# Kernel tuning notes

Hardware: AMD Instinct MI355X
Metric: run time of the kernel (lower is better)

## Reference

```python
import jax, jax.numpy as jnp
import numpy as np

HEAD_DIM = 64
N_HEADS = 12
N_KV_HEADS = 4
N_REP = N_HEADS // N_KV_HEADS  # 3


def _rope(x, cos, sin):
    # x: [B, S, H, D]; cos/sin: [1, S, D//2] -> broadcast over heads
    x2 = x.reshape(*x.shape[:-1], -1, 2)          # [B,S,H,D/2,2]
    x_r, x_i = x2[..., 0], x2[..., 1]
    c = cos[:, :, None, :]                         # [1,S,1,D/2]
    s = sin[:, :, None, :]
    o_r = x_r * c - x_i * s
    o_i = x_r * s + x_i * c
    return jnp.stack([o_r, o_i], axis=-1).reshape(x.shape)


def setup_inputs() -> dict:
    key = jax.random.key(0)
    ks = jax.random.split(key, 6)
    B, S, H = 4, 2048, 768
    hidden_state = jax.random.normal(ks[0], (B, S, H), dtype=jnp.float32)
    # true RoPE frequencies (theta=10000) for positions 0..S-1
    inv_freq = 1.0 / (10000.0 ** (np.arange(0, HEAD_DIM, 2, dtype=np.float32) / HEAD_DIM))
    ang = np.arange(S, dtype=np.float32)[:, None] * inv_freq[None, :]  # [S, D/2]
    freqs_cos = jnp.asarray(np.cos(ang))[None]     # [1,S,32]
    freqs_sin = jnp.asarray(np.sin(ang))[None]
    sc = 0.02
    wq = jax.random.normal(ks[1], (768, 768), dtype=jnp.float32) * sc
    wk = jax.random.normal(ks[2], (256, 768), dtype=jnp.float32) * sc
    wv = jax.random.normal(ks[3], (256, 768), dtype=jnp.float32) * sc
    wo = jax.random.normal(ks[4], (768, 768), dtype=jnp.float32) * sc
    return {"hidden_state": hidden_state, "freqs_cos": freqs_cos, "freqs_sin": freqs_sin,
            "wq": wq, "wk": wk, "wv": wv, "wo": wo}


def reference(hidden_state, freqs_cos, freqs_sin, wq, wk, wv, wo):
    B, S, _ = hidden_state.shape
    q = (hidden_state @ wq.T).reshape(B, S, N_HEADS, HEAD_DIM)
    k = (hidden_state @ wk.T).reshape(B, S, N_KV_HEADS, HEAD_DIM)
    v = (hidden_state @ wv.T).reshape(B, S, N_KV_HEADS, HEAD_DIM)
    q = _rope(q, freqs_cos, freqs_sin)
    k = _rope(k, freqs_cos, freqs_sin)
    # repeat_kv: [B,S,KV,D] -> [B,S,KV*n_rep,D]
    k = jnp.repeat(k, N_REP, axis=2)
    v = jnp.repeat(v, N_REP, axis=2)
    q = q.transpose(0, 2, 1, 3)  # [B,H,S,D]
    k = k.transpose(0, 2, 1, 3)
    v = v.transpose(0, 2, 1, 3)
    scores = jnp.einsum('bhqd,bhkd->bhqk', q, k) / np.sqrt(HEAD_DIM).astype(np.float32)
    mask = jnp.triu(jnp.full((S, S), -jnp.inf, dtype=scores.dtype), k=1)
    scores = scores + mask
    attn = jax.nn.softmax(scores.astype(jnp.float32), axis=-1).astype(q.dtype)
    # dropout is inference-off (identity)
    out = jnp.einsum('bhqk,bhkd->bhqd', attn, v)
    out = out.transpose(0, 2, 1, 3).reshape(B, S, N_HEADS * HEAD_DIM)
    return out @ wo.T, attn
```

## Files before the change

kernel.cpp:

```cpp
#include <hip/hip_runtime.h>
#include <hip/hip_bf16.h>
#include <stdint.h>


typedef __bf16 bf16x8 __attribute__((ext_vector_type(8)));
typedef float  f32x4  __attribute__((ext_vector_type(4)));

#define B_    4
#define S_    2048
#define H_    768
#define NH_Q  12
#define NKV_  4
#define D_    64
#define MROWS (B_ * S_)
#define NQKV  1280

__device__ __forceinline__ f32x4 mfma16(bf16x8 a, bf16x8 b, f32x4 c) {
  return __builtin_amdgcn_mfma_f32_16x16x32_bf16(a, b, c, 0, 0, 0);
}

__device__ __forceinline__ void st_nt4(float* p, f32x4 v) {
  __builtin_nontemporal_store(v, (f32x4*)p);
}

__device__ __forceinline__ uint32_t pk2(float a, float b) {
  __bf16 x = (__bf16)a, y = (__bf16)b;
  uint16_t xu = __builtin_bit_cast(uint16_t, x);
  uint16_t yu = __builtin_bit_cast(uint16_t, y);
  return (uint32_t)xu | ((uint32_t)yu << 16);
}
__device__ __forceinline__ float bl(uint32_t u) {
  uint32_t t = u << 16; return __builtin_bit_cast(float, t);
}
__device__ __forceinline__ float bh(uint32_t u) {
  uint32_t t = u & 0xffff0000u; return __builtin_bit_cast(float, t);
}

__global__ void cast_bf16_kernel(const float* __restrict__ s, __bf16* __restrict__ d, int n8) {
  int i = blockIdx.x * 256 + threadIdx.x;
  if (i >= n8) return;
  const float4* sp = (const float4*)s + (size_t)i * 2;
  float4 a = sp[0], b = sp[1];
  bf16x8 o;
  o[0] = (__bf16)a.x; o[1] = (__bf16)a.y; o[2] = (__bf16)a.z; o[3] = (__bf16)a.w;
  o[4] = (__bf16)b.x; o[5] = (__bf16)b.y; o[6] = (__bf16)b.z; o[7] = (__bf16)b.w;
  *((bf16x8*)d + i) = o;
}

__global__ __launch_bounds__(256) void gemm_qkv(const __bf16* __restrict__ A,
                                                const __bf16* __restrict__ Wq,
                                                const __bf16* __restrict__ Wk,
                                                const __bf16* __restrict__ Wv,
                                                float* __restrict__ C) {
  const int K = 768;
  __shared__ __bf16 As[128 * 32];
  __shared__ __bf16 Bs[128 * 32];
  const int m0 = blockIdx.x * 128, n0 = blockIdx.y * 128;
  const __bf16* W;
  int nl;
  if (n0 < 768)       { W = Wq; nl = n0; }
  else if (n0 < 1024) { W = Wk; nl = n0 - 768; }
  else                { W = Wv; nl = n0 - 1024; }
  const int tid = threadIdx.x, lane = tid & 63, w = tid >> 6;
  const int wm = w >> 1, wn = w & 1;
  const int ql = lane & 15, grp = lane >> 4;
  const int srow = tid >> 1, shalf = tid & 1;
  const int sw = (srow >> 1) & 3;
  const int kc0 = (shalf * 2) ^ sw, kc1 = (shalf * 2 + 1) ^ sw;

  f32x4 acc[4][4] = {};

  for (int k0 = 0; k0 < K; k0 += 32) {
    bf16x8 av0 = *(const bf16x8*)(A + (size_t)(m0 + srow) * K + k0 + shalf * 16);
    bf16x8 av1 = *(const bf16x8*)(A + (size_t)(m0 + srow) * K + k0 + shalf * 16 + 8);
    bf16x8 bv0 = *(const bf16x8*)(W + (size_t)(nl + srow) * K + k0 + shalf * 16);
    bf16x8 bv1 = *(const bf16x8*)(W + (size_t)(nl + srow) * K + k0 + shalf * 16 + 8);
    __syncthreads();
    *(bf16x8*)(As + srow * 32 + kc0 * 8) = av0;
    *(bf16x8*)(As + srow * 32 + kc1 * 8) = av1;
    *(bf16x8*)(Bs + srow * 32 + kc0 * 8) = bv0;
    *(bf16x8*)(Bs + srow * 32 + kc1 * 8) = bv1;
    __syncthreads();

    bf16x8 af[4], bf_[4];
#pragma unroll
    for (int i = 0; i < 4; i++) {
      int row = wm * 64 + i * 16 + ql;
      int kc = grp ^ ((row >> 1) & 3);
      af[i] = *(const bf16x8*)(As + row * 32 + kc * 8);
    }
#pragma unroll
    for (int j = 0; j < 4; j++) {
      int row = wn * 64 + j * 16 + ql;
      int kc = grp ^ ((row >> 1) & 3);
      bf_[j] = *(const bf16x8*)(Bs + row * 32 + kc * 8);
    }
#pragma unroll
    for (int i = 0; i < 4; i++)
#pragma unroll
      for (int j = 0; j < 4; j++)
        acc[i][j] = mfma16(af[i], bf_[j], acc[i][j]);
  }

#pragma unroll
  for (int i = 0; i < 4; i++)
#pragma unroll
    for (int j = 0; j < 4; j++)
#pragma unroll
      for (int r = 0; r < 4; r++) {
        int row = m0 + wm * 64 + i * 16 + grp * 4 + r;
        int col = n0 + wn * 64 + j * 16 + ql;
        C[(size_t)row * NQKV + col] = acc[i][j][r];
      }
}

__global__ __launch_bounds__(256) void gemm_xwT(const __bf16* __restrict__ A,
                                                const __bf16* __restrict__ W,
                                                float* __restrict__ C,
                                                int M, int N, int K) {
  __shared__ __bf16 As[128 * 32];
  __shared__ __bf16 Bs[128 * 32];
  const int m0 = blockIdx.x * 128, n0 = blockIdx.y * 128;
  const int tid = threadIdx.x, lane = tid & 63, w = tid >> 6;
  const int wm = w >> 1, wn = w & 1;
  const int ql = lane & 15, grp = lane >> 4;
  const int srow = tid >> 1, shalf = tid & 1;
  const int sw = (srow >> 1) & 3;
  const int kc0 = (shalf * 2) ^ sw, kc1 = (shalf * 2 + 1) ^ sw;

  f32x4 acc[4][4] = {};

  for (int k0 = 0; k0 < K; k0 += 32) {
    bf16x8 av0 = *(const bf16x8*)(A + (size_t)(m0 + srow) * K + k0 + shalf * 16);
    bf16x8 av1 = *(const bf16x8*)(A + (size_t)(m0 + srow) * K + k0 + shalf * 16 + 8);
    bf16x8 bv0 = *(const bf16x8*)(W + (size_t)(n0 + srow) * K + k0 + shalf * 16);
    bf16x8 bv1 = *(const bf16x8*)(W + (size_t)(n0 + srow) * K + k0 + shalf * 16 + 8);
    __syncthreads();
    *(bf16x8*)(As + srow * 32 + kc0 * 8) = av0;
    *(bf16x8*)(As + srow * 32 + kc1 * 8) = av1;
    *(bf16x8*)(Bs + srow * 32 + kc0 * 8) = bv0;
    *(bf16x8*)(Bs + srow * 32 + kc1 * 8) = bv1;
    __syncthreads();

    bf16x8 af[4], bf_[4];
#pragma unroll
    for (int i = 0; i < 4; i++) {
      int row = wm * 64 + i * 16 + ql;
      int kc = grp ^ ((row >> 1) & 3);
      af[i] = *(const bf16x8*)(As + row * 32 + kc * 8);
    }
#pragma unroll
    for (int j = 0; j < 4; j++) {
      int row = wn * 64 + j * 16 + ql;
      int kc = grp ^ ((row >> 1) & 3);
      bf_[j] = *(const bf16x8*)(Bs + row * 32 + kc * 8);
    }
#pragma unroll
    for (int i = 0; i < 4; i++)
#pragma unroll
      for (int j = 0; j < 4; j++)
        acc[i][j] = mfma16(af[i], bf_[j], acc[i][j]);
  }

#pragma unroll
  for (int i = 0; i < 4; i++)
#pragma unroll
    for (int j = 0; j < 4; j++)
#pragma unroll
      for (int r = 0; r < 4; r++) {
        int row = m0 + wm * 64 + i * 16 + grp * 4 + r;
        int col = n0 + wn * 64 + j * 16 + ql;
        C[(size_t)row * N + col] = acc[i][j][r];
      }
}

template <int NH>
__global__ void rope_pack(const float* __restrict__ src, int colOff, int stride,
                          const float* __restrict__ fc, const float* __restrict__ fs,
                          __bf16* __restrict__ dst, float scale) {
  int idx = blockIdx.x * 256 + threadIdx.x;
  const int total = MROWS * NH * 32;
  if (idx >= total) return;
  int t = idx & 31;
  int h = (idx >> 5) % NH;
  int row = idx / (32 * NH);
  int s = row & (S_ - 1), b = row >> 11;
  float x0 = src[(size_t)row * stride + colOff + h * 64 + 2 * t];
  float x1 = src[(size_t)row * stride + colOff + h * 64 + 2 * t + 1];
  float c = fc[s * 32 + t], sn = fs[s * 32 + t];
  float o0 = (x0 * c - x1 * sn) * scale;
  float o1 = (x0 * sn + x1 * c) * scale;
  __bf16* d = dst + (((size_t)(b * NH + h) * S_ + s) * 64 + 2 * t);
  d[0] = (__bf16)o0;
  d[1] = (__bf16)o1;
}

__global__ void transpose_v(const float* __restrict__ QKV, __bf16* __restrict__ VT) {
  __shared__ float tile[64][65];
  int rt = blockIdx.x;
  int ct = blockIdx.y;
  int r0 = rt * 64, c0 = ct * 64;
  int tx = threadIdx.x & 63, ty = threadIdx.x >> 6;
#pragma unroll
  for (int rep = 0; rep < 16; rep++) {
    int rr = rep * 4 + ty;
    tile[rr][tx] = QKV[(size_t)(r0 + rr) * NQKV + 1024 + c0 + tx];
  }
  __syncthreads();
  int b = r0 >> 11;
  int s0 = r0 & (S_ - 1);
#pragma unroll
  for (int rep = 0; rep < 16; rep++) {
    int dr = rep * 4 + ty;
    int d = c0 + dr;
    int kv = d >> 6, dd = d & 63;
    VT[(((size_t)(b * NKV_ + kv) * 64 + dd) * S_) + s0 + tx] = (__bf16)tile[tx][dr];
  }
}

template <int MAXC>
__device__ __forceinline__ void attn_part(
    int g, int b, int h, int w, int lane,
    const __bf16* __restrict__ Q, const __bf16* __restrict__ Kp,
    const __bf16* __restrict__ Vp, float* __restrict__ attn,
    __bf16* __restrict__ O, float (*lsum_s)[16], f32x4 (*obuf)[4]) {
  const int ql = lane & 15, grp = lane >> 4;
  const int qr0 = g * 16;
  const int nch = (g >> 1) + 1;
  const int i_q = qr0 + ql;
  const __bf16* Qp = Q + ((size_t)(b * NH_Q + h) * S_ + qr0) * 64;
  float* attnp = attn + ((size_t)(b * NH_Q + h) * S_ + qr0) * S_;

  bf16x8 bq0 = *(const bf16x8*)(Qp + ql * 64 + grp * 8);
  bf16x8 bq1 = *(const bf16x8*)(Qp + ql * 64 + 32 + grp * 8);

  uint32_t p[MAXC][4];
  float lsum = 0.f;

#pragma unroll
  for (int c = 0; c < MAXC; c++) {
    const int j = w + 4 * c;
    if (j < nch) {
      const int j0 = j * 32;
      bf16x8 k0 = *(const bf16x8*)(Kp + (size_t)(j0 + ql) * 64 + grp * 8);
      bf16x8 k1 = *(const bf16x8*)(Kp + (size_t)(j0 + ql) * 64 + 32 + grp * 8);
      bf16x8 k2 = *(const bf16x8*)(Kp + (size_t)(j0 + 16 + ql) * 64 + grp * 8);
      bf16x8 k3 = *(const bf16x8*)(Kp + (size_t)(j0 + 16 + ql) * 64 + 32 + grp * 8);
      f32x4 s0 = {}, s1 = {};
      s0 = mfma16(k0, bq0, s0);
      s0 = mfma16(k1, bq1, s0);
      s1 = mfma16(k2, bq0, s1);
      s1 = mfma16(k3, bq1, s1);
      float e[8];
      if (j == nch - 1) {
#pragma unroll
        for (int r = 0; r < 4; r++) {
          int ja = j0 + grp * 4 + r, jb = j0 + 16 + grp * 4 + r;
          e[r]     = (ja <= i_q) ? exp2f(s0[r]) : 0.f;
          e[4 + r] = (jb <= i_q) ? exp2f(s1[r]) : 0.f;
        }
      } else {
#pragma unroll
        for (int r = 0; r < 4; r++) {
          e[r]     = exp2f(s0[r]);
          e[4 + r] = exp2f(s1[r]);
        }
      }
#pragma unroll
      for (int r = 0; r < 8; r++) lsum += e[r];
      p[c][0] = pk2(e[0], e[1]);
      p[c][1] = pk2(e[2], e[3]);
      p[c][2] = pk2(e[4], e[5]);
      p[c][3] = pk2(e[6], e[7]);
    }
  }

  lsum += __shfl_xor(lsum, 16);
  lsum += __shfl_xor(lsum, 32);
  if (lane < 16) lsum_s[w][ql] = lsum;
  __syncthreads();
  const float rinv = 1.f / (lsum_s[0][ql] + lsum_s[1][ql] + lsum_s[2][ql] + lsum_s[3][ql]);

  f32x4 opv[4] = {};
#pragma unroll
  for (int c = 0; c < MAXC; c++) {
    const int j = w + 4 * c;
    if (j < nch) {
      const int j0 = j * 32;
      bf16x8 v0 = *(const bf16x8*)(Vp + (size_t)(0 * 16 + ql) * S_ + j0 + grp * 8);
      bf16x8 v1 = *(const bf16x8*)(Vp + (size_t)(1 * 16 + ql) * S_ + j0 + grp * 8);
      bf16x8 v2 = *(const bf16x8*)(Vp + (size_t)(2 * 16 + ql) * S_ + j0 + grp * 8);
      bf16x8 v3 = *(const bf16x8*)(Vp + (size_t)(3 * 16 + ql) * S_ + j0 + grp * 8);

      f32x4 q0, q1;
      q0[0] = bl(p[c][0]); q0[1] = bh(p[c][0]); q0[2] = bl(p[c][1]); q0[3] = bh(p[c][1]);
      q1[0] = bl(p[c][2]); q1[1] = bh(p[c][2]); q1[2] = bl(p[c][3]); q1[3] = bh(p[c][3]);
#pragma unroll
      for (int r = 0; r < 4; r++) { q0[r] *= rinv; q1[r] *= rinv; }
      st_nt4(attnp + (size_t)ql * S_ + j0 + grp * 4, q0);
      st_nt4(attnp + (size_t)ql * S_ + j0 + 16 + grp * 4, q1);

      int srcA = ql + 32 * (grp & 1);
      int srcB = srcA + 16;
      uint32_t A0 = __shfl(p[c][0], srcA), A1 = __shfl(p[c][1], srcA);
      uint32_t A2 = __shfl(p[c][2], srcA), A3 = __shfl(p[c][3], srcA);
      uint32_t B0 = __shfl(p[c][0], srcB), B1 = __shfl(p[c][1], srcB);
      uint32_t B2 = __shfl(p[c][2], srcB), B3 = __shfl(p[c][3], srcB);
      bool hi = (grp >> 1) != 0;
      union { bf16x8 v; uint32_t u[4]; } pu;
      pu.u[0] = hi ? A2 : A0;
      pu.u[1] = hi ? A3 : A1;
      pu.u[2] = hi ? B2 : B0;
      pu.u[3] = hi ? B3 : B1;
      opv[0] = mfma16(pu.v, v0, opv[0]);
      opv[1] = mfma16(pu.v, v1, opv[1]);
      opv[2] = mfma16(pu.v, v2, opv[2]);
      opv[3] = mfma16(pu.v, v3, opv[3]);
    }
  }

  f32x4* ob = obuf[w * 64 + lane];
  ob[0] = opv[0]; ob[1] = opv[1]; ob[2] = opv[2]; ob[3] = opv[3];
  __syncthreads();
  {
    const int dt = w;
    f32x4 acc = obuf[0 * 64 + lane][dt];
    acc += obuf[1 * 64 + lane][dt];
    acc += obuf[2 * 64 + lane][dt];
    acc += obuf[3 * 64 + lane][dt];
    __bf16* Op = O + ((size_t)(b * S_) + qr0) * H_ + h * 64;
#pragma unroll
    for (int r = 0; r < 4; r++) {
      int row = grp * 4 + r;
      float rr = 1.f / (lsum_s[0][row] + lsum_s[1][row] + lsum_s[2][row] + lsum_s[3][row]);
      Op[(size_t)row * H_ + dt * 16 + ql] = (__bf16)(acc[r] * rr);
    }
  }

  const int jz = nch * 32;
  const int tid = w * 64 + lane;
  const f32x4 z4 = {0.f, 0.f, 0.f, 0.f};
#pragma unroll 1
  for (int rr = 0; rr < 16; rr++) {
    float* rowp = attnp + (size_t)rr * S_;
    for (int jj = jz + tid * 4; jj < S_; jj += 1024) st_nt4(rowp + jj, z4);
  }
  __syncthreads();
}

__global__ __launch_bounds__(256) void attn_kernel(const __bf16* __restrict__ Q,
                                                   const __bf16* __restrict__ Kb,
                                                   const __bf16* __restrict__ VT,
                                                   float* __restrict__ attn,
                                                   __bf16* __restrict__ O) {
  __shared__ float lsum_s[4][16];
  __shared__ f32x4 obuf[4 * 64][4];
  const int x = blockIdx.x, h = blockIdx.y, b = blockIdx.z;
  const int lane = threadIdx.x & 63, w = threadIdx.x >> 6;
  const int kv = h / 3;
  const __bf16* Kp = Kb + (size_t)(b * NKV_ + kv) * S_ * 64;
  const __bf16* Vp = VT + (size_t)(b * NKV_ + kv) * 64 * S_;

  attn_part<8>(x, b, h, w, lane, Q, Kp, Vp, attn, O, lsum_s, obuf);
  attn_part<16>(127 - x, b, h, w, lane, Q, Kp, Vp, attn, O, lsum_s, obuf);
}

extern "C" void kernel_launch(void* const* d_in, const int* in_sizes, int n_in,
                              void* d_out, int out_size, void* d_ws, size_t ws_size,
                              hipStream_t stream) {
  (void)in_sizes; (void)n_in;
  const float* X  = (const float*)d_in[0];
  const float* fc = (const float*)d_in[1];
  const float* fs = (const float*)d_in[2];
  const float* wq = (const float*)d_in[3];
  const float* wk = (const float*)d_in[4];
  const float* wv = (const float*)d_in[5];
  const float* wo = (const float*)d_in[6];
  float* out0 = (float*)d_out;
  float* attn = out0 + (size_t)B_ * S_ * H_;

  char* p = (char*)d_ws;
  auto take = [&](size_t bytes) -> char* {
    char* r = p;
    p += (bytes + 255) & ~(size_t)255;
    return r;
  };
  __bf16* wqbf = (__bf16*)take((size_t)768 * 768 * 2);
  __bf16* wkbf = (__bf16*)take((size_t)256 * 768 * 2);
  __bf16* wvbf = (__bf16*)take((size_t)256 * 768 * 2);
  __bf16* wobf = (__bf16*)take((size_t)768 * 768 * 2);
  __bf16* Qbf  = (__bf16*)take((size_t)MROWS * 768 * 2);
  __bf16* Kbf  = (__bf16*)take((size_t)MROWS * 256 * 2);
  __bf16* VTbf = (__bf16*)take((size_t)MROWS * 256 * 2);
  __bf16* Obf  = (__bf16*)take((size_t)MROWS * 768 * 2);
  size_t used = (size_t)(p - (char*)d_ws);

  const size_t XBF_B  = (size_t)MROWS * 768 * 2;
  const size_t QKV_B  = (size_t)MROWS * NQKV * 4;
  const size_t TEMP_B = XBF_B + QKV_B;

  char* tp;
  if (used + TEMP_B + 1024 <= ws_size) {
    tp = p;
  } else {
    tp = (char*)(((uintptr_t)((char*)d_out + (size_t)out_size * 4 - TEMP_B)) & ~(uintptr_t)255);
  }
  __bf16* Xbf  = (__bf16*)tp;  tp += XBF_B;
  float*  QKVf = (float*)tp;

  {
    int n8;
    n8 = (MROWS * 768) / 8;
    cast_bf16_kernel<<<(n8 + 255) / 256, 256, 0, stream>>>(X, Xbf, n8);
    n8 = (768 * 768) / 8;
    cast_bf16_kernel<<<(n8 + 255) / 256, 256, 0, stream>>>(wq, wqbf, n8);
    cast_bf16_kernel<<<(n8 + 255) / 256, 256, 0, stream>>>(wo, wobf, n8);
    n8 = (256 * 768) / 8;
    cast_bf16_kernel<<<(n8 + 255) / 256, 256, 0, stream>>>(wk, wkbf, n8);
    cast_bf16_kernel<<<(n8 + 255) / 256, 256, 0, stream>>>(wv, wvbf, n8);
  }

  gemm_qkv<<<dim3(MROWS / 128, NQKV / 128), 256, 0, stream>>>(Xbf, wqbf, wkbf, wvbf, QKVf);

  rope_pack<NH_Q><<<(MROWS * NH_Q * 32) / 256, 256, 0, stream>>>(QKVf, 0, NQKV, fc, fs, Qbf, 0.125f * 1.44269504f);
  rope_pack<NKV_><<<(MROWS * NKV_ * 32) / 256, 256, 0, stream>>>(QKVf, 768, NQKV, fc, fs, Kbf, 1.0f);
  transpose_v<<<dim3(MROWS / 64, 4), 256, 0, stream>>>(QKVf, VTbf);

  attn_kernel<<<dim3(64, NH_Q, B_), 256, 0, stream>>>(Qbf, Kbf, VTbf, attn, Obf);

  gemm_xwT<<<dim3(MROWS / 128, 768 / 128), 256, 0, stream>>>(Obf, wobf, out0, MROWS, 768, 768);
}
```

Measured before the change: 314.9 us.

## Use direct global-to-LDS loads in GEMMs and drop shuffles in PV MFMA

```diff
diff --git a/kernel.cpp b/kernel.cpp
--- a/kernel.cpp
+++ b/kernel.cpp
@@ -5,6 +5,7 @@
 
 typedef __bf16 bf16x8 __attribute__((ext_vector_type(8)));
 typedef float  f32x4  __attribute__((ext_vector_type(4)));
+typedef uint32_t u32x2 __attribute__((ext_vector_type(2)));
 
 #define B_    4
 #define S_    2048
@@ -34,6 +35,12 @@
 }
 __device__ __forceinline__ float bh(uint32_t u) {
   uint32_t t = u & 0xffff0000u; return __builtin_bit_cast(float, t);
+}
+
+__device__ __forceinline__ void gload_lds16(const __bf16* g, __bf16* l) {
+  __builtin_amdgcn_global_load_lds(
+      (const __attribute__((address_space(1))) void*)g,
+      (__attribute__((address_space(3))) void*)l, 16, 0, 0);
 }
 
 __global__ void cast_bf16_kernel(const float* __restrict__ s, __bf16* __restrict__ d, int n8) {
@@ -47,12 +54,84 @@
   *((bf16x8*)d + i) = o;
 }
 
+struct GemmPtrs {
+  const __bf16 *gA0, *gA1, *gB0, *gB1;
+};
+__device__ __forceinline__ void gemm_core(GemmPtrs gp, int K,
+                                          __bf16* As, __bf16* Bs,
+                                          int tid, f32x4 (*acc)[4]) {
+  const int lane = tid & 63, w = tid >> 6;
+  const int wm = w >> 1, wn = w & 1;
+  const int ql = lane & 15, grp = lane >> 4;
+  __bf16* lA0 = As + (size_t)(tid & ~63) * 8;
+  __bf16* lA1 = lA0 + 256 * 8;
+  __bf16* lB0 = Bs + (size_t)(tid & ~63) * 8;
+  __bf16* lB1 = lB0 + 256 * 8;
+
+  for (int k0 = 0; k0 < K; k0 += 32) {
+    gload_lds16(gp.gA0 + k0, lA0);
+    gload_lds16(gp.gA1 + k0, lA1);
+    gload_lds16(gp.gB0 + k0, lB0);
+    gload_lds16(gp.gB1 + k0, lB1);
+    __syncthreads();
+
+    bf16x8 af[4], bf_[4];
+#pragma unroll
+    for (int i = 0; i < 4; i++) {
+      int row = wm * 64 + i * 16 + ql;
+      int kc = grp ^ ((row >> 1) & 3);
+      af[i] = *(const bf16x8*)(As + row * 32 + kc * 8);
+    }
+#pragma unroll
+    for (int j = 0; j < 4; j++) {
+      int row = wn * 64 + j * 16 + ql;
+      int kc = grp ^ ((row >> 1) & 3);
+      bf_[j] = *(const bf16x8*)(Bs + row * 32 + kc * 8);
+    }
+#pragma unroll
+    for (int i = 0; i < 4; i++)
+#pragma unroll
+      for (int j = 0; j < 4; j++)
+        acc[i][j] = mfma16(af[i], bf_[j], acc[i][j]);
+    __syncthreads();
+  }
+}
+
+__device__ __forceinline__ GemmPtrs make_ptrs(const __bf16* A, const __bf16* W,
+                                              int m0, int n0, int K, int tid) {
+  GemmPtrs gp;
+  int c0 = tid, c1 = 256 + tid;
+  int sr0 = c0 >> 2, kc0 = (c0 & 3) ^ ((sr0 >> 1) & 3);
+  int sr1 = c1 >> 2, kc1 = (c1 & 3) ^ ((sr1 >> 1) & 3);
+  gp.gA0 = A + (size_t)(m0 + sr0) * K + kc0 * 8;
+  gp.gA1 = A + (size_t)(m0 + sr1) * K + kc1 * 8;
+  gp.gB0 = W + (size_t)(n0 + sr0) * K + kc0 * 8;
+  gp.gB1 = W + (size_t)(n0 + sr1) * K + kc1 * 8;
+  return gp;
+}
+
+__device__ __forceinline__ void gemm_store(f32x4 (*acc)[4], float* C, int M, int N,
+                                           int m0, int n0, int tid) {
+  const int lane = tid & 63, w = tid >> 6;
+  const int wm = w >> 1, wn = w & 1;
+  const int ql = lane & 15, grp = lane >> 4;
+#pragma unroll
+  for (int i = 0; i < 4; i++)
+#pragma unroll
+    for (int j = 0; j < 4; j++)
+#pragma unroll
+      for (int r = 0; r < 4; r++) {
+        int row = m0 + wm * 64 + i * 16 + grp * 4 + r;
+        int col = n0 + wn * 64 + j * 16 + ql;
+        C[(size_t)row * N + col] = acc[i][j][r];
+      }
+}
+
 __global__ __launch_bounds__(256) void gemm_qkv(const __bf16* __restrict__ A,
                                                 const __bf16* __restrict__ Wq,
                                                 const __bf16* __restrict__ Wk,
                                                 const __bf16* __restrict__ Wv,
                                                 float* __restrict__ C) {
-  const int K = 768;
   __shared__ __bf16 As[128 * 32];
   __shared__ __bf16 Bs[128 * 32];
   const int m0 = blockIdx.x * 128, n0 = blockIdx.y * 128;
@@ -61,57 +140,11 @@
   if (n0 < 768)       { W = Wq; nl = n0; }
   else if (n0 < 1024) { W = Wk; nl = n0 - 768; }
   else                { W = Wv; nl = n0 - 1024; }
-  const int tid = threadIdx.x, lane = tid & 63, w = tid >> 6;
-  const int wm = w >> 1, wn = w & 1;
-  const int ql = lane & 15, grp = lane >> 4;
-  const int srow = tid >> 1, shalf = tid & 1;
-  const int sw = (srow >> 1) & 3;
-  const int kc0 = (shalf * 2) ^ sw, kc1 = (shalf * 2 + 1) ^ sw;
-
+  const int tid = threadIdx.x;
   f32x4 acc[4][4] = {};
-
-  for (int k0 = 0; k0 < K; k0 += 32) {
-    bf16x8 av0 = *(const bf16x8*)(A + (size_t)(m0 + srow) * K + k0 + shalf * 16);
-    bf16x8 av1 = *(const bf16x8*)(A + (size_t)(m0 + srow) * K + k0 + shalf * 16 + 8);
-    bf16x8 bv0 = *(const bf16x8*)(W + (size_t)(nl + srow) * K + k0 + shalf * 16);
-    bf16x8 bv1 = *(const bf16x8*)(W + (size_t)(nl + srow) * K + k0 + shalf * 16 + 8);
-    __syncthreads();
-    *(bf16x8*)(As + srow * 32 + kc0 * 8) = av0;
-    *(bf16x8*)(As + srow * 32 + kc1 * 8) = av1;
-    *(bf16x8*)(Bs + srow * 32 + kc0 * 8) = bv0;
-    *(bf16x8*)(Bs + srow * 32 + kc1 * 8) = bv1;
-    __syncthreads();
-
-    bf16x8 af[4], bf_[4];
-#pragma unroll
-    for (int i = 0; i < 4; i++) {
-      int row = wm * 64 + i * 16 + ql;
-      int kc = grp ^ ((row >> 1) & 3);
-      af[i] = *(const bf16x8*)(As + row * 32 + kc * 8);
-    }
-#pragma unroll
-    for (int j = 0; j < 4; j++) {
-      int row = wn * 64 + j * 16 + ql;
-      int kc = grp ^ ((row >> 1) & 3);
-      bf_[j] = *(const bf16x8*)(Bs + row * 32 + kc * 8);
-    }
-#pragma unroll
-    for (int i = 0; i < 4; i++)
-#pragma unroll
-      for (int j = 0; j < 4; j++)
-        acc[i][j] = mfma16(af[i], bf_[j], acc[i][j]);
-  }
-
-#pragma unroll
-  for (int i = 0; i < 4; i++)
-#pragma unroll
-    for (int j = 0; j < 4; j++)
-#pragma unroll
-      for (int r = 0; r < 4; r++) {
-        int row = m0 + wm * 64 + i * 16 + grp * 4 + r;
-        int col = n0 + wn * 64 + j * 16 + ql;
-        C[(size_t)row * NQKV + col] = acc[i][j][r];
-      }
+  GemmPtrs gp = make_ptrs(A, W, m0, nl, 768, tid);
+  gemm_core(gp, 768, As, Bs, tid, acc);
+  gemm_store(acc, C, MROWS, NQKV, m0, n0, tid);
 }
 
 __global__ __launch_bounds__(256) void gemm_xwT(const __bf16* __restrict__ A,
@@ -121,57 +154,11 @@
   __shared__ __bf16 As[128 * 32];
   __shared__ __bf16 Bs[128 * 32];
   const int m0 = blockIdx.x * 128, n0 = blockIdx.y * 128;
-  const int tid = threadIdx.x, lane = tid & 63, w = tid >> 6;
-  const int wm = w >> 1, wn = w & 1;
-  const int ql = lane & 15, grp = lane >> 4;
-  const int srow = tid >> 1, shalf = tid & 1;
-  const int sw = (srow >> 1) & 3;
-  const int kc0 = (shalf * 2) ^ sw, kc1 = (shalf * 2 + 1) ^ sw;
-
+  const int tid = threadIdx.x;
   f32x4 acc[4][4] = {};
-
-  for (int k0 = 0; k0 < K; k0 += 32) {
-    bf16x8 av0 = *(const bf16x8*)(A + (size_t)(m0 + srow) * K + k0 + shalf * 16);
-    bf16x8 av1 = *(const bf16x8*)(A + (size_t)(m0 + srow) * K + k0 + shalf * 16 + 8);
-    bf16x8 bv0 = *(const bf16x8*)(W + (size_t)(n0 + srow) * K + k0 + shalf * 16);
-    bf16x8 bv1 = *(const bf16x8*)(W + (size_t)(n0 + srow) * K + k0 + shalf * 16 + 8);
-    __syncthreads();
-    *(bf16x8*)(As + srow * 32 + kc0 * 8) = av0;
-    *(bf16x8*)(As + srow * 32 + kc1 * 8) = av1;
-    *(bf16x8*)(Bs + srow * 32 + kc0 * 8) = bv0;
-    *(bf16x8*)(Bs + srow * 32 + kc1 * 8) = bv1;
-    __syncthreads();
-
-    bf16x8 af[4], bf_[4];
-#pragma unroll
-    for (int i = 0; i < 4; i++) {
-      int row = wm * 64 + i * 16 + ql;
-      int kc = grp ^ ((row >> 1) & 3);
-      af[i] = *(const bf16x8*)(As + row * 32 + kc * 8);
-    }
-#pragma unroll
-    for (int j = 0; j < 4; j++) {
-      int row = wn * 64 + j * 16 + ql;
-      int kc = grp ^ ((row >> 1) & 3);
-      bf_[j] = *(const bf16x8*)(Bs + row * 32 + kc * 8);
-    }
-#pragma unroll
-    for (int i = 0; i < 4; i++)
-#pragma unroll
-      for (int j = 0; j < 4; j++)
-        acc[i][j] = mfma16(af[i], bf_[j], acc[i][j]);
-  }
-
-#pragma unroll
-  for (int i = 0; i < 4; i++)
-#pragma unroll
-    for (int j = 0; j < 4; j++)
-#pragma unroll
-      for (int r = 0; r < 4; r++) {
-        int row = m0 + wm * 64 + i * 16 + grp * 4 + r;
-        int col = n0 + wn * 64 + j * 16 + ql;
-        C[(size_t)row * N + col] = acc[i][j][r];
-      }
+  GemmPtrs gp = make_ptrs(A, W, m0, n0, K, tid);
+  gemm_core(gp, K, As, Bs, tid, acc);
+  gemm_store(acc, C, M, N, m0, n0, tid);
 }
 
 template <int NH>
@@ -287,10 +274,18 @@
     const int j = w + 4 * c;
     if (j < nch) {
       const int j0 = j * 32;
-      bf16x8 v0 = *(const bf16x8*)(Vp + (size_t)(0 * 16 + ql) * S_ + j0 + grp * 8);
-      bf16x8 v1 = *(const bf16x8*)(Vp + (size_t)(1 * 16 + ql) * S_ + j0 + grp * 8);
-      bf16x8 v2 = *(const bf16x8*)(Vp + (size_t)(2 * 16 + ql) * S_ + j0 + grp * 8);
-      bf16x8 v3 = *(const bf16x8*)(Vp + (size_t)(3 * 16 + ql) * S_ + j0 + grp * 8);
+      union { bf16x8 v; uint32_t u[4]; } av;
+      av.u[0] = p[c][0]; av.u[1] = p[c][1]; av.u[2] = p[c][2]; av.u[3] = p[c][3];
+      const __bf16* vb0 = Vp + j0 + 4 * grp;
+      const __bf16* vb1 = vb0 + 16;
+#pragma unroll
+      for (int dt = 0; dt < 4; dt++) {
+        const size_t ro = (size_t)(dt * 16 + ql) * S_;
+        union { bf16x8 v; u32x2 h[2]; } bv;
+        bv.h[0] = *(const u32x2*)(vb0 + ro);
+        bv.h[1] = *(const u32x2*)(vb1 + ro);
+        opv[dt] = mfma16(av.v, bv.v, opv[dt]);
+      }
 
       f32x4 q0, q1;
       q0[0] = bl(p[c][0]); q0[1] = bh(p[c][0]); q0[2] = bl(p[c][1]); q0[3] = bh(p[c][1]);
@@ -299,23 +294,6 @@
       for (int r = 0; r < 4; r++) { q0[r] *= rinv; q1[r] *= rinv; }
       st_nt4(attnp + (size_t)ql * S_ + j0 + grp * 4, q0);
       st_nt4(attnp + (size_t)ql * S_ + j0 + 16 + grp * 4, q1);
-
-      int srcA = ql + 32 * (grp & 1);
-      int srcB = srcA + 16;
-      uint32_t A0 = __shfl(p[c][0], srcA), A1 = __shfl(p[c][1], srcA);
-      uint32_t A2 = __shfl(p[c][2], srcA), A3 = __shfl(p[c][3], srcA);
-      uint32_t B0 = __shfl(p[c][0], srcB), B1 = __shfl(p[c][1], srcB);
-      uint32_t B2 = __shfl(p[c][2], srcB), B3 = __shfl(p[c][3], srcB);
-      bool hi = (grp >> 1) != 0;
-      union { bf16x8 v; uint32_t u[4]; } pu;
-      pu.u[0] = hi ? A2 : A0;
-      pu.u[1] = hi ? A3 : A1;
-      pu.u[2] = hi ? B2 : B0;
-      pu.u[3] = hi ? B3 : B1;
-      opv[0] = mfma16(pu.v, v0, opv[0]);
-      opv[1] = mfma16(pu.v, v1, opv[1]);
-      opv[2] = mfma16(pu.v, v2, opv[2]);
-      opv[3] = mfma16(pu.v, v3, opv[3]);
     }
   }
 
```

Measured after the change: 398.3 us. +26.5%, slower.
